# Performance work log

Hardware: AMD Instinct MI355X
Metric: run time of the kernel (lower is better)

Reference implementation:

```python
import jax, jax.numpy as jnp
import numpy as np

C = 256; Ca = C // 2; WH = 8; WW = 8; K = 3; NH = 8; HD = Ca // NH
EPS_LN = 1e-5; EPS_BN = 1e-5

def _rel_pos_idx(wh, ww):
    coords = np.stack(np.meshgrid(np.arange(wh), np.arange(ww), indexing='ij'))  # (2,wh,ww)
    flat = coords.reshape(2, -1)
    rel = (flat[:, :, None] - flat[:, None, :]).transpose(1, 2, 0).astype(np.int64)  # (N,N,2)
    rel[..., 0] += wh - 1
    rel[..., 1] += ww - 1
    rel[..., 0] *= 2 * ww - 1
    return jnp.asarray(rel.sum(-1))  # (N,N)

REL_IDX = _rel_pos_idx(WH, WW)

def _ln(x, g, b):
    m = x.mean(-1, keepdims=True)
    v = x.var(-1, keepdims=True)
    return (x - m) / jnp.sqrt(v + EPS_LN) * g + b

def _bn(x, g, b):  # eval-mode BN, running_mean=0, running_var=1; x is NCHW
    return x * (g / np.sqrt(1.0 + EPS_BN))[None, :, None, None] + b[None, :, None, None]

def _conv1x1(x, w, b):  # w: (O, I)
    return jnp.einsum('bchw,oc->bohw', x, w) + b[None, :, None, None]

def _rwp(x, h, w, wh, ww):  # windows (B*nW, wh*ww, c) -> image (B, c, h, w)
    Bn, N, c = x.shape
    nh, nw = h // wh, w // ww
    B = Bn // (nh * nw)
    x = x.reshape(B, nh, nw, wh, ww, c)
    return x.transpose(0, 5, 1, 3, 2, 4).reshape(B, c, h, w)

def _wp(x, wh, ww):  # image (B, c, h, w) -> windows (B*nW, wh*ww, c)
    B, c, h, w = x.shape
    x = x.reshape(B, c, h // wh, wh, w // ww, ww)
    return x.transpose(0, 2, 4, 3, 5, 1).reshape(-1, wh * ww, c)

def _gelu(t):
    return jax.nn.gelu(t, approximate=False)

def forward(x, rel_pos_bias, attn_w, attn_b, attn_ln_g, attn_ln_b,
            conv_w, conv_b, conv_bn_g, conv_bn_b,
            ci_w1, ci_b1, ci_bn_g, ci_bn_b, ci_w2, ci_b2,
            pr_w, pr_b, cn_bn_g, cn_bn_b,
            qkv_w, qkv_b,
            si_w1, si_b1, si_bn_g, si_bn_b, si_w2, si_b2,
            an_g, an_b, out_w, out_b, h, w):
    B_, N, Cfull = x.shape
    x_attn = _ln(x @ attn_w + attn_b, attn_ln_g, attn_ln_b)  # (B_, N, Ca)
    # conv branch -- note: source applies RWP to raw x (proj_cnn output is dead code)
    x_img = _rwp(x, h, w, WH, WW)  # (B, C, h, w)
    pad = K // 2
    x_cnn = jax.lax.conv_general_dilated(
        x_img, conv_w, (1, 1), [(pad, pad), (pad, pad)],
        dimension_numbers=('NCHW', 'OIHW', 'NCHW'), feature_group_count=Cfull)
    x_cnn = _gelu(_bn(x_cnn + conv_b[None, :, None, None], conv_bn_g, conv_bn_b))
    gap = x_cnn.mean((2, 3), keepdims=True)  # (B, C, 1, 1)
    ci = _conv1x1(gap, ci_w1, ci_b1)
    ci = _gelu(_bn(ci, ci_bn_g, ci_bn_b))
    ci = _conv1x1(ci, ci_w2, ci_b2)  # (B, Ca, 1, 1)
    x_cnn = _conv1x1(x_cnn, pr_w, pr_b)  # (B, Ca, h, w)
    # windowed attention
    qkv = (x_attn @ qkv_w + qkv_b).reshape(B_, N, 3, NH, HD).transpose(2, 0, 3, 1, 4)
    q, k, v = qkv[0], qkv[1], qkv[2]  # each (B_, NH, N, HD)
    B = ci.shape[0]
    ci_s = jax.nn.sigmoid(ci).reshape(B, 1, NH, 1, HD)
    v = (v.reshape(B, B_ // B, NH, N, HD) * ci_s).reshape(B_, NH, N, HD)
    scale = HD ** -0.5
    attn = jnp.einsum('bhnd,bhmd->bhnm', q * scale, k)
    bias = rel_pos_bias[REL_IDX]  # (N, N, NH)
    attn = jax.nn.softmax(attn + bias.transpose(2, 0, 1)[None], axis=-1)
    x_attn = jnp.einsum('bhnm,bhmd->bhnd', attn, v).transpose(0, 2, 1, 3).reshape(B_, N, Ca)
    # spatial interaction gating of conv branch
    x_sp = _rwp(x_attn, h, w, WH, WW)  # (B, Ca, h, w)
    si = _conv1x1(x_sp, si_w1, si_b1)
    si = _gelu(_bn(si, si_bn_g, si_bn_b))
    si = _conv1x1(si, si_w2, si_b2)  # (B, 1, h, w)
    x_cnn = jax.nn.sigmoid(si * x_cnn)
    x_cnn = _bn(x_cnn, cn_bn_g, cn_bn_b)
    x_cnn = _wp(x_cnn, WH, WW)  # (B_, N, Ca)
    x_attn = _ln(x_attn, an_g, an_b)
    return jnp.concatenate([x_attn, x_cnn], axis=-1) @ out_w + out_b

def setup_inputs() -> dict:
    key = jax.random.key(0)
    ks = jax.random.split(key, 12)
    B_, N = 2048, WH * WW
    s = 0.02
    return dict(
        x=jax.random.normal(ks[0], (B_, N, C), jnp.float32),
        rel_pos_bias=jax.random.uniform(ks[1], ((2 * WH - 1) * (2 * WW - 1), NH), jnp.float32),
        attn_w=jax.random.normal(ks[2], (C, Ca)) * s, attn_b=jnp.zeros((Ca,)),
        attn_ln_g=jnp.ones((Ca,)), attn_ln_b=jnp.zeros((Ca,)),
        conv_w=jax.random.normal(ks[3], (C, 1, K, K)) * s, conv_b=jnp.zeros((C,)),
        conv_bn_g=jnp.ones((C,)), conv_bn_b=jnp.zeros((C,)),
        ci_w1=jax.random.normal(ks[4], (C // 8, C)) * s, ci_b1=jnp.zeros((C // 8,)),
        ci_bn_g=jnp.ones((C // 8,)), ci_bn_b=jnp.zeros((C // 8,)),
        ci_w2=jax.random.normal(ks[5], (Ca, C // 8)) * s, ci_b2=jnp.zeros((Ca,)),
        pr_w=jax.random.normal(ks[6], (Ca, C)) * s, pr_b=jnp.zeros((Ca,)),
        cn_bn_g=jnp.ones((Ca,)), cn_bn_b=jnp.zeros((Ca,)),
        qkv_w=jax.random.normal(ks[7], (Ca, 3 * Ca)) * s, qkv_b=jnp.zeros((3 * Ca,)),
        si_w1=jax.random.normal(ks[8], (C // 16, Ca)) * s, si_b1=jnp.zeros((C // 16,)),
        si_bn_g=jnp.ones((C // 16,)), si_bn_b=jnp.zeros((C // 16,)),
        si_w2=jax.random.normal(ks[9], (1, C // 16)) * s, si_b2=jnp.zeros((1,)),
        an_g=jnp.ones((Ca,)), an_b=jnp.zeros((Ca,)),
        out_w=jax.random.normal(ks[10], (C, C)) * s, out_b=jnp.zeros((C,)),
        h=64, w=64,
    )

def reference(x, rel_pos_bias, attn_w, attn_b, attn_ln_g, attn_ln_b,
              conv_w, conv_b, conv_bn_g, conv_bn_b,
              ci_w1, ci_b1, ci_bn_g, ci_bn_b, ci_w2, ci_b2,
              pr_w, pr_b, cn_bn_g, cn_bn_b,
              qkv_w, qkv_b,
              si_w1, si_b1, si_bn_g, si_bn_b, si_w2, si_b2,
              an_g, an_b, out_w, out_b, h, w):
    return forward(x, rel_pos_bias, attn_w, attn_b, attn_ln_g, attn_ln_b,
                   conv_w, conv_b, conv_bn_g, conv_bn_b,
                   ci_w1, ci_b1, ci_bn_g, ci_bn_b, ci_w2, ci_b2,
                   pr_w, pr_b, cn_bn_g, cn_bn_b,
                   qkv_w, qkv_b,
                   si_w1, si_b1, si_bn_g, si_bn_b, si_w2, si_b2,
                   an_g, an_b, out_w, out_b, h, w)
```

## Files before the change

### kernel.cpp

```cpp
#include <hip/hip_runtime.h>
#include <math.h>


#define BNR 0.9999950000374998f

typedef __attribute__((ext_vector_type(8))) short short8;
typedef __attribute__((ext_vector_type(4))) float f32x4;
typedef __attribute__((ext_vector_type(4))) _Float16 half4;
typedef __attribute__((ext_vector_type(8))) _Float16 half8;
typedef __attribute__((ext_vector_type(2))) _Float16 h2v;

__device__ __forceinline__ float gelu_f(float x) {
  const float z = x * (1.0f + 0.044715f * x * x);
  return x / (1.0f + __expf(-1.5957691216057308f * z));
}
__device__ __forceinline__ unsigned short f2bf(float f) {
  unsigned int u = __builtin_bit_cast(unsigned int, f);
  u += 0x7fffu + ((u >> 16) & 1u);
  return (unsigned short)(u >> 16);
}
__device__ __forceinline__ float bf2f(unsigned short h) {
  unsigned int u = ((unsigned int)h) << 16;
  return __builtin_bit_cast(float, u);
}
__device__ __forceinline__ void ld8(const unsigned short* p, float* o) {
  const short8 v = *(const short8*)p;
#pragma unroll
  for (int i = 0; i < 8; ++i) o[i] = bf2f((unsigned short)v[i]);
}
__device__ __forceinline__ unsigned int pkh(float a, float b) {
  return __builtin_bit_cast(unsigned int, __builtin_amdgcn_cvt_pkrtz(a, b));
}

#define ATI(r, ch) (((r) << 8) + ((((ch) ^ ((r)&7))) << 3))

__global__ __launch_bounds__(256) void kpack(
    const float* __restrict__ aw, const float* __restrict__ qw,
    const float* __restrict__ prw, const float* __restrict__ ow,
    const float* __restrict__ sw1, unsigned short* __restrict__ awp,
    unsigned short* __restrict__ qwp, unsigned short* __restrict__ prwp,
    unsigned short* __restrict__ owp, unsigned short* __restrict__ sw1p) {
  const int b = blockIdx.x;
  const float* src; unsigned short* dst; int fs, K, N, NT, trans, f16o;
  if (b < 64)       { fs = b;       src = aw;  dst = awp;  K = 256; N = 128; NT = 8;  trans = 0; f16o = 0; }
  else if (b < 160) { fs = b - 64;  src = qw;  dst = qwp;  K = 128; N = 384; NT = 24; trans = 0; f16o = 0; }
  else if (b < 224) { fs = b - 160; src = prw; dst = prwp; K = 256; N = 128; NT = 8;  trans = 1; f16o = 1; }
  else if (b < 352) { fs = b - 224; src = ow;  dst = owp;  K = 256; N = 256; NT = 16; trans = 0; f16o = 0; }
  else              { fs = b - 352; src = sw1; dst = sw1p; K = 128; N = 16;  NT = 1;  trans = 1; f16o = 0; }
  const int ks = fs / NT, nt = fs % NT;
  for (int idx = threadIdx.x; idx < 512; idx += 256) {
    const int l = idx >> 3, i = idx & 7;
    const int k = ks * 32 + ((l >> 4) << 3) + i, n = nt * 16 + (l & 15);
    const float v = trans ? src[n * K + k] : src[k * N + n];
    dst[(fs * 64 + l) * 8 + i] =
        f16o ? __builtin_bit_cast(unsigned short, (_Float16)v) : f2bf(v);
  }
}

__global__ __launch_bounds__(256) void kbias(const float* __restrict__ rpb,
                                             unsigned short* __restrict__ bt) {
  const int i = blockIdx.x * 256 + threadIdx.x;
  const int h = i >> 12, n = (i >> 6) & 63, m = i & 63;
  const int ny = n >> 3, nx = n & 7, my = m >> 3, mx = m & 7;
  const float v = rpb[((ny - my + 7) * 15 + (nx - mx + 7)) * 8 + h];
  bt[i] = __builtin_bit_cast(unsigned short, (_Float16)v);
}

__global__ __launch_bounds__(256) void k1_attn_ln(
    const float* __restrict__ x, const unsigned short* __restrict__ awp,
    const float* __restrict__ ab, const float* __restrict__ lg,
    const float* __restrict__ lb, unsigned short* __restrict__ xattn,
    unsigned short* __restrict__ xb) {
  const int tid = threadIdx.x, w = tid >> 6, l = tid & 63;
  const int lr = l & 15, lg4 = l >> 4;
  const int r0 = blockIdx.x * 64 + w * 16;
  const float* xp = x + (size_t)(r0 + lr) * 256 + lg4 * 8;
  unsigned short* xbp = xb + (size_t)(r0 + lr) * 256 + lg4 * 8;
  short8 a[8];
#pragma unroll
  for (int ks = 0; ks < 8; ++ks) {
    const float4 f0 = *(const float4*)(xp + ks * 32);
    const float4 f1 = *(const float4*)(xp + ks * 32 + 4);
    short8 av;
    av[0] = f2bf(f0.x); av[1] = f2bf(f0.y); av[2] = f2bf(f0.z); av[3] = f2bf(f0.w);
    av[4] = f2bf(f1.x); av[5] = f2bf(f1.y); av[6] = f2bf(f1.z); av[7] = f2bf(f1.w);
    a[ks] = av;
    uint4 hv;
    hv.x = pkh(f0.x, f0.y); hv.y = pkh(f0.z, f0.w);
    hv.z = pkh(f1.x, f1.y); hv.w = pkh(f1.z, f1.w);
    *(uint4*)(xbp + ks * 32) = hv;
  }
  f32x4 acc[8];
#pragma unroll
  for (int nt = 0; nt < 8; ++nt) acc[nt] = (f32x4)0.f;
#pragma unroll
  for (int nt = 0; nt < 8; ++nt)
#pragma unroll
    for (int ks = 0; ks < 8; ++ks) {
      const short8 bfr = *(const short8*)(awp + ((ks * 8 + nt) * 64 + l) * 8);
      acc[nt] = __builtin_amdgcn_mfma_f32_16x16x32_bf16(a[ks], bfr, acc[nt], 0, 0, 0);
    }
  float bias[8], gam[8], bet[8];
#pragma unroll
  for (int nt = 0; nt < 8; ++nt) {
    const int col = nt * 16 + lr;
    bias[nt] = ab[col]; gam[nt] = lg[col]; bet[nt] = lb[col];
  }
#pragma unroll
  for (int j = 0; j < 4; ++j) {
    float s = 0.f, qq = 0.f;
#pragma unroll
    for (int nt = 0; nt < 8; ++nt) {
      const float v = acc[nt][j] + bias[nt];
      acc[nt][j] = v; s += v; qq += v * v;
    }
    s += __shfl_xor(s, 1); s += __shfl_xor(s, 2);
    s += __shfl_xor(s, 4); s += __shfl_xor(s, 8);
    qq += __shfl_xor(qq, 1); qq += __shfl_xor(qq, 2);
    qq += __shfl_xor(qq, 4); qq += __shfl_xor(qq, 8);
    const float mean = s * (1.f / 128.f);
    const float var = qq * (1.f / 128.f) - mean * mean;
    const float rstd = rsqrtf(var + 1e-5f);
    const int row = r0 + lg4 * 4 + j;
#pragma unroll
    for (int nt = 0; nt < 8; ++nt)
      xattn[(size_t)row * 128 + nt * 16 + lr] =
          f2bf((acc[nt][j] - mean) * rstd * gam[nt] + bet[nt]);
  }
}

__global__ __launch_bounds__(256) void k25_conv(
    const unsigned short* __restrict__ xb, const float* __restrict__ cw,
    const float* __restrict__ cb, const float* __restrict__ bg,
    const float* __restrict__ bb, const unsigned short* __restrict__ prwp,
    const float* __restrict__ prb, unsigned short* __restrict__ xpr,
    float* __restrict__ gpart) {
  __shared__ unsigned short gl[32][264];
  const int tid = threadIdx.x;
  const int bid = (blockIdx.x & 7) * 512 + (blockIdx.x >> 3);
  const int b = bid >> 7;
  const int y = (bid >> 1) & 63;
  const int xt = (bid & 1) * 32;
  const int w = tid >> 6, l = tid & 63;
  {
    const int c0 = l << 2;
    h2v w01[9], w23[9];
#pragma unroll
    for (int k = 0; k < 9; ++k) {
      w01[k][0] = (_Float16)cw[(c0 + 0) * 9 + k];
      w01[k][1] = (_Float16)cw[(c0 + 1) * 9 + k];
      w23[k][0] = (_Float16)cw[(c0 + 2) * 9 + k];
      w23[k][1] = (_Float16)cw[(c0 + 3) * 9 + k];
    }
    const float4 cbf = *(const float4*)&cb[c0];
    float4 scf = *(const float4*)&bg[c0];
    scf.x *= BNR; scf.y *= BNR; scf.z *= BNR; scf.w *= BNR;
    const float4 sbf = *(const float4*)&bb[c0];
    h2v cb01 = {(_Float16)cbf.x, (_Float16)cbf.y};
    h2v cb23 = {(_Float16)cbf.z, (_Float16)cbf.w};
    h2v sc01 = {(_Float16)scf.x, (_Float16)scf.y};
    h2v sc23 = {(_Float16)scf.z, (_Float16)scf.w};
    h2v sb01 = {(_Float16)sbf.x, (_Float16)sbf.y};
    h2v sb23 = {(_Float16)sbf.z, (_Float16)sbf.w};
    float4 gsum = make_float4(0.f, 0.f, 0.f, 0.f);
    const int px0 = xt + w * 8;
#pragma unroll
    for (int sc2 = 0; sc2 < 2; ++sc2) {
      const int p0 = px0 + sc2 * 4;
      h2v v0[3][6], v1[3][6];
#pragma unroll
      for (int dy = 0; dy < 3; ++dy) {
        const int yy = y + dy - 1;
        const bool vy = (unsigned)yy < 64u;
        const int ybase = vy ? ((b * 64 + (yy >> 3) * 8) * 64 + (yy & 7) * 8) : 0;
#pragma unroll
        for (int q = 0; q < 6; ++q) {
          const int xx = p0 - 1 + q;
          h2v a = (h2v)(_Float16)0.f, c = (h2v)(_Float16)0.f;
          if (vy && (unsigned)xx < 64u) {
            const int row = ybase + (xx >> 3) * 64 + (xx & 7);
            const uint2 u = *(const uint2*)&xb[(size_t)row * 256 + c0];
            a = __builtin_bit_cast(h2v, u.x);
            c = __builtin_bit_cast(h2v, u.y);
          }
          v0[dy][q] = a; v1[dy][q] = c;
        }
      }
#pragma unroll
      for (int p = 0; p < 4; ++p) {
        h2v s0 = cb01, s1 = cb23;
#pragma unroll
        for (int dy = 0; dy < 3; ++dy)
#pragma unroll
          for (int dx = 0; dx < 3; ++dx) {
            s0 = w01[dy * 3 + dx] * v0[dy][p + dx] + s0;
            s1 = w23[dy * 3 + dx] * v1[dy][p + dx] + s1;
          }
        s0 = s0 * sc01 + sb01;
        s1 = s1 * sc23 + sb23;
        const float g0 = gelu_f((float)s0[0]), g1 = gelu_f((float)s0[1]);
        const float g2 = gelu_f((float)s1[0]), g3 = gelu_f((float)s1[1]);
        uint2 pk;
        pk.x = pkh(g0, g1); pk.y = pkh(g2, g3);
        *(uint2*)&gl[w * 8 + sc2 * 4 + p][c0] = pk;
        gsum.x += g0; gsum.y += g1; gsum.z += g2; gsum.w += g3;
      }
    }
    *(float4*)&gpart[(size_t)bid * 256 + c0] = gsum;
  }
  __syncthreads();
  const int lr = l & 15, lg4 = l >> 4;
  const int mr0 = (w & 1) * 16, nt0 = (w >> 1) * 4;
  half8 a[8];
#pragma unroll
  for (int ks = 0; ks < 8; ++ks)
    a[ks] = __builtin_bit_cast(half8,
                               *(const short8*)&gl[mr0 + lr][ks * 32 + lg4 * 8]);
  f32x4 acc[4];
#pragma unroll
  for (int nt = 0; nt < 4; ++nt) acc[nt] = (f32x4)0.f;
#pragma unroll
  for (int nt = 0; nt < 4; ++nt)
#pragma unroll
    for (int ks = 0; ks < 8; ++ks) {
      const half8 bfr = __builtin_bit_cast(
          half8, *(const short8*)(prwp + ((ks * 8 + nt0 + nt) * 64 + l) * 8));
      acc[nt] = __builtin_amdgcn_mfma_f32_16x16x32_f16(a[ks], bfr, acc[nt], 0, 0, 0);
    }
#pragma unroll
  for (int nt = 0; nt < 4; ++nt) {
    const int col = (nt0 + nt) * 16 + lr;
    const float bv = prb[col];
#pragma unroll
    for (int j = 0; j < 4; ++j) {
      const int pix = (b * 64 + y) * 64 + xt + mr0 + lg4 * 4 + j;
      xpr[(size_t)pix * 128 + col] = f2bf(acc[nt][j] + bv);
    }
  }
}

__global__ __launch_bounds__(128) void k3_ci(
    const float* __restrict__ gp, const float* __restrict__ w1,
    const float* __restrict__ b1, const float* __restrict__ g1,
    const float* __restrict__ bb1, const float* __restrict__ w2,
    const float* __restrict__ b2, float* __restrict__ cis) {
  __shared__ float gm[256];
  __shared__ float c1[32];
  const int b = blockIdx.x, tid = threadIdx.x;
  for (int c = tid; c < 256; c += 128) {
    float s = 0.f;
    for (int p = 0; p < 128; ++p) s += gp[(size_t)(b * 128 + p) * 256 + c];
    gm[c] = s * (1.f / 4096.f);
  }
  __syncthreads();
  if (tid < 32) {
    float s = b1[tid];
    for (int c = 0; c < 256; ++c) s = fmaf(gm[c], w1[tid * 256 + c], s);
    s = s * (g1[tid] * BNR) + bb1[tid];
    c1[tid] = gelu_f(s);
  }
  __syncthreads();
  float s = b2[tid];
#pragma unroll
  for (int i = 0; i < 32; ++i) s = fmaf(c1[i], w2[tid * 32 + i], s);
  cis[b * 128 + tid] = 1.f / (1.f + __expf(-s));
}

__global__ __launch_bounds__(256, 4) void k4_attn(
    const unsigned short* __restrict__ xa, const unsigned short* __restrict__ qwp,
    const float* __restrict__ qb, const float* __restrict__ cis,
    const unsigned short* __restrict__ biasT, unsigned short* __restrict__ attn) {
  __shared__ _Float16 QS[4][64][38];
  __shared__ _Float16 KS[4][64][38];
  const int tid = threadIdx.x;
  const int win = blockIdx.x, img = win >> 6;
  const int w = tid >> 6, l = tid & 63, lr = l & 15, lg4 = l >> 4;
  {
    float qbv[4];
#pragma unroll
    for (int t = 0; t < 4; ++t) {
      const int gnt = (t < 2) ? (2 * w + t) : (8 + 2 * w + t - 2);
      qbv[t] = qb[gnt * 16 + lr];
    }
    f32x4 acc[4][4];
#pragma unroll
    for (int mt = 0; mt < 4; ++mt)
#pragma unroll
      for (int t = 0; t < 4; ++t) acc[mt][t] = (f32x4)0.f;
#pragma unroll
    for (int ks = 0; ks < 4; ++ks) {
      short8 a[4];
#pragma unroll
      for (int mt = 0; mt < 4; ++mt)
        a[mt] = *(const short8*)(xa + (size_t)(win * 64 + mt * 16 + lr) * 128 +
                                 ks * 32 + lg4 * 8);
#pragma unroll
      for (int t = 0; t < 4; ++t) {
        const int gnt = (t < 2) ? (2 * w + t) : (8 + 2 * w + t - 2);
        const short8 bfr = *(const short8*)(qwp + ((ks * 24 + gnt) * 64 + l) * 8);
#pragma unroll
        for (int mt = 0; mt < 4; ++mt)
          acc[mt][t] = __builtin_amdgcn_mfma_f32_16x16x32_bf16(a[mt], bfr,
                                                               acc[mt][t], 0, 0, 0);
      }
    }
#pragma unroll
    for (int mt = 0; mt < 4; ++mt)
#pragma unroll
      for (int t = 0; t < 4; ++t)
#pragma unroll
        for (int j = 0; j < 4; ++j) {
          const int row = mt * 16 + lg4 * 4 + j;
          const float v = acc[mt][t][j] + qbv[t];
          if (t < 2) QS[w][row][t * 16 + lr] = (_Float16)(v * 0.25f);
          else KS[w][row][(t - 2) * 16 + lr] = (_Float16)v;
        }
  }
  half4 bV2[2][4];
  {
    float qbv[2], cisv[2];
#pragma unroll
    for (int t = 0; t < 2; ++t) {
      qbv[t] = qb[(16 + 2 * w + t) * 16 + lr];
      cisv[t] = cis[img * 128 + (2 * w + t) * 16 + lr];
    }
    f32x4 accv[4][2];
#pragma unroll
    for (int mt = 0; mt < 4; ++mt)
#pragma unroll
      for (int t = 0; t < 2; ++t) accv[mt][t] = (f32x4)0.f;
#pragma unroll
    for (int ks = 0; ks < 4; ++ks) {
      short8 a[4];
#pragma unroll
      for (int mt = 0; mt < 4; ++mt)
        a[mt] = *(const short8*)(xa + (size_t)(win * 64 + mt * 16 + lr) * 128 +
                                 ks * 32 + lg4 * 8);
#pragma unroll
      for (int t = 0; t < 2; ++t) {
        const short8 bfr =
            *(const short8*)(qwp + ((ks * 24 + 16 + 2 * w + t) * 64 + l) * 8);
#pragma unroll
        for (int mt = 0; mt < 4; ++mt)
          accv[mt][t] = __builtin_amdgcn_mfma_f32_16x16x32_bf16(a[mt], bfr,
                                                                accv[mt][t], 0, 0, 0);
      }
    }
#pragma unroll
    for (int t = 0; t < 2; ++t)
#pragma unroll
      for (int kt = 0; kt < 4; ++kt) {
        half4 p;
#pragma unroll
        for (int i = 0; i < 4; ++i)
          p[i] = (_Float16)((accv[kt][t][i] + qbv[t]) * cisv[t]);
        bV2[t][kt] = p;
      }
  }
  for (int hi = 0; hi < 2; ++hi) {
    const int h = w * 2 + hi;
    half4 aK[4], bQ[4];
#pragma unroll
    for (int mt = 0; mt < 4; ++mt)
      aK[mt] = *(const half4*)&KS[w][mt * 16 + lr][hi * 16 + lg4 * 4];
#pragma unroll
    for (int nt = 0; nt < 4; ++nt)
      bQ[nt] = *(const half4*)&QS[w][nt * 16 + lr][hi * 16 + lg4 * 4];
    f32x4 s[4][4];
#pragma unroll
    for (int mt = 0; mt < 4; ++mt)
#pragma unroll
      for (int nt = 0; nt < 4; ++nt)
        s[mt][nt] = __builtin_amdgcn_mfma_f32_16x16x16f16(aK[mt], bQ[nt],
                                                          (f32x4)0.f, 0, 0, 0);
#pragma unroll
    for (int nt = 0; nt < 4; ++nt) {
      const int n = nt * 16 + lr;
      const unsigned short* bp = biasT + (((h << 6) + n) << 6);
#pragma unroll
      for (int mt = 0; mt < 4; ++mt) {
        const half4 b4 = *(const half4*)(bp + mt * 16 + lg4 * 4);
        s[mt][nt][0] += (float)b4[0];
        s[mt][nt][1] += (float)b4[1];
        s[mt][nt][2] += (float)b4[2];
        s[mt][nt][3] += (float)b4[3];
      }
    }
    float inv[4];
#pragma unroll
    for (int nt = 0; nt < 4; ++nt) {
      float m0 = -1e30f;
#pragma unroll
      for (int mt = 0; mt < 4; ++mt)
#pragma unroll
        for (int r = 0; r < 4; ++r) m0 = fmaxf(m0, s[mt][nt][r]);
      m0 = fmaxf(m0, __shfl_xor(m0, 16));
      m0 = fmaxf(m0, __shfl_xor(m0, 32));
      float d0 = 0.f;
#pragma unroll
      for (int mt = 0; mt < 4; ++mt)
#pragma unroll
        for (int r = 0; r < 4; ++r) {
          const float e = __expf(s[mt][nt][r] - m0);
          s[mt][nt][r] = e;
          d0 += e;
        }
      d0 += __shfl_xor(d0, 16);
      d0 += __shfl_xor(d0, 32);
      inv[nt] = 1.f / d0;
    }
    half4 pa[4][4];
#pragma unroll
    for (int nt = 0; nt < 4; ++nt)
#pragma unroll
      for (int kt = 0; kt < 4; ++kt) {
        half4 p;
#pragma unroll
        for (int r = 0; r < 4; ++r) p[r] = (_Float16)(s[kt][nt][r] * inv[nt]);
        pa[nt][kt] = p;
      }
    f32x4 o[4];
#pragma unroll
    for (int nt = 0; nt < 4; ++nt) o[nt] = (f32x4)0.f;
#pragma unroll
    for (int nt = 0; nt < 4; ++nt)
#pragma unroll
      for (int kt = 0; kt < 4; ++kt)
        o[nt] = __builtin_amdgcn_mfma_f32_16x16x16f16(pa[nt][kt], bV2[hi][kt],
                                                      o[nt], 0, 0, 0);
#pragma unroll
    for (int nt = 0; nt < 4; ++nt)
#pragma unroll
      for (int r = 0; r < 4; ++r) {
        const int token = win * 64 + nt * 16 + lg4 * 4 + r;
        attn[(size_t)token * 128 + h * 16 + lr] = f2bf(o[nt][r]);
      }
  }
}

__global__ __launch_bounds__(256) void k6_tail(
    const unsigned short* __restrict__ attn, const unsigned short* __restrict__ xpr,
    const unsigned short* __restrict__ sw1p, const float* __restrict__ sb1,
    const float* __restrict__ sgc, const float* __restrict__ sbc,
    const float* __restrict__ sw2, const float* __restrict__ sb2,
    const float* __restrict__ cg, const float* __restrict__ cbb,
    const float* __restrict__ ag, const float* __restrict__ abb,
    const unsigned short* __restrict__ owp, const float* __restrict__ ob,
    float* __restrict__ out) {
  __shared__ unsigned short At[64 * 256];
  __shared__ float sifl[64];
  __shared__ float statl[64][2];
  const int tid = threadIdx.x;
  const int R0 = blockIdx.x * 64;
  const int w = tid >> 6, l = tid & 63, lr = l & 15, lg4 = l >> 4;
  for (int i = tid; i < 1024; i += 256) {
    const int r = i >> 4, c16 = i & 15;
    *(uint4*)&At[ATI(r, c16)] =
        *(const uint4*)&attn[(size_t)(R0 + r) * 128 + c16 * 8];
    const int R = R0 + r, win = R >> 6, tt = R & 63;
    const int bimg = win >> 6, wy = (win >> 3) & 7, wx = win & 7;
    const int pix = (bimg * 64 + wy * 8 + (tt >> 3)) * 64 + wx * 8 + (tt & 7);
    *(uint4*)&At[ATI(r, 16 + c16)] =
        *(const uint4*)&xpr[(size_t)pix * 128 + c16 * 8];
  }
  __syncthreads();
  {
    const int r = tid >> 2, q = tid & 3;
    float xv[32];
#pragma unroll
    for (int b8 = 0; b8 < 4; ++b8) ld8(&At[ATI(r, q * 4 + b8)], xv + b8 * 8);
    float ps = 0.f, pq = 0.f;
#pragma unroll
    for (int j = 0; j < 32; ++j) { ps += xv[j]; pq += xv[j] * xv[j]; }
    ps += __shfl_xor(ps, 1); ps += __shfl_xor(ps, 2);
    pq += __shfl_xor(pq, 1); pq += __shfl_xor(pq, 2);
    if (q == 0) {
      const float mean = ps * (1.f / 128.f);
      const float var = pq * (1.f / 128.f) - mean * mean;
      statl[r][0] = mean;
      statl[r][1] = rsqrtf(var + 1e-5f);
    }
  }
  {
    const int row = w * 16 + lr;
    f32x4 sa = (f32x4)0.f;
#pragma unroll
    for (int ks = 0; ks < 4; ++ks) {
      const short8 a4 = *(const short8*)&At[ATI(row, ks * 4 + lg4)];
      const short8 bfr = *(const short8*)(sw1p + (ks * 64 + l) * 8);
      sa = __builtin_amdgcn_mfma_f32_16x16x32_bf16(a4, bfr, sa, 0, 0, 0);
    }
    const float sb1v = sb1[lr], g1v = sgc[lr] * BNR, b1v = sbc[lr];
    const float w2v = sw2[lr], sb2v = sb2[0];
#pragma unroll
    for (int j = 0; j < 4; ++j) {
      float s = (sa[j] + sb1v) * g1v + b1v;
      float p = gelu_f(s) * w2v;
      p += __shfl_xor(p, 1); p += __shfl_xor(p, 2);
      p += __shfl_xor(p, 4); p += __shfl_xor(p, 8);
      if (lr == 0) sifl[w * 16 + lg4 * 4 + j] = p + sb2v;
    }
  }
  __syncthreads();
  {
    const int c = tid & 127;
    const float agv = ag[c], abbv = abb[c];
    const float cgv = cg[c] * BNR, cbbv = cbb[c];
#pragma unroll
    for (int k = 0; k < 32; ++k) {
      const int r = (tid >> 7) + k * 2;
      const int ia = ATI(r, c >> 3) + (c & 7);
      const int ic = ATI(r, 16 + (c >> 3)) + (c & 7);
      float a = bf2f(At[ia]);
      a = (a - statl[r][0]) * statl[r][1] * agv + abbv;
      At[ia] = f2bf(a);
      const float cv = bf2f(At[ic]);
      const float g = 1.f / (1.f + __expf(-sifl[r] * cv));
      At[ic] = f2bf(g * cgv + cbbv);
    }
  }
  __syncthreads();
  const int row = w * 16 + lr;
  short8 a[8];
#pragma unroll
  for (int ks = 0; ks < 8; ++ks)
    a[ks] = *(const short8*)&At[ATI(row, ks * 4 + lg4)];
  f32x4 acc[16];
#pragma unroll
  for (int nt = 0; nt < 16; ++nt) acc[nt] = (f32x4)0.f;
#pragma unroll
  for (int nt = 0; nt < 16; ++nt)
#pragma unroll
    for (int ks = 0; ks < 8; ++ks) {
      const short8 bfr = *(const short8*)(owp + ((ks * 16 + nt) * 64 + l) * 8);
      acc[nt] = __builtin_amdgcn_mfma_f32_16x16x32_bf16(a[ks], bfr, acc[nt], 0, 0, 0);
    }
#pragma unroll
  for (int nt = 0; nt < 16; ++nt) {
    const int col = nt * 16 + lr;
    const float bv = ob[col];
#pragma unroll
    for (int j = 0; j < 4; ++j)
      out[(size_t)(R0 + w * 16 + lg4 * 4 + j) * 256 + col] = acc[nt][j] + bv;
  }
}

extern "C" void kernel_launch(void* const* d_in, const int* in_sizes, int n_in,
                              void* d_out, int out_size, void* d_ws,
                              size_t ws_size, hipStream_t stream) {
  (void)in_sizes; (void)n_in; (void)out_size; (void)ws_size;
  const float* x      = (const float*)d_in[0];
  const float* rpb    = (const float*)d_in[1];
  const float* attn_w = (const float*)d_in[2];
  const float* attn_b = (const float*)d_in[3];
  const float* aln_g  = (const float*)d_in[4];
  const float* aln_b  = (const float*)d_in[5];
  const float* conv_w = (const float*)d_in[6];
  const float* conv_b = (const float*)d_in[7];
  const float* cbn_g  = (const float*)d_in[8];
  const float* cbn_b  = (const float*)d_in[9];
  const float* ci_w1  = (const float*)d_in[10];
  const float* ci_b1  = (const float*)d_in[11];
  const float* ci_bg  = (const float*)d_in[12];
  const float* ci_bb  = (const float*)d_in[13];
  const float* ci_w2  = (const float*)d_in[14];
  const float* ci_b2  = (const float*)d_in[15];
  const float* pr_w   = (const float*)d_in[16];
  const float* pr_b   = (const float*)d_in[17];
  const float* cn_g   = (const float*)d_in[18];
  const float* cn_b   = (const float*)d_in[19];
  const float* qkv_w  = (const float*)d_in[20];
  const float* qkv_b  = (const float*)d_in[21];
  const float* si_w1  = (const float*)d_in[22];
  const float* si_b1  = (const float*)d_in[23];
  const float* si_bg  = (const float*)d_in[24];
  const float* si_bb  = (const float*)d_in[25];
  const float* si_w2  = (const float*)d_in[26];
  const float* si_b2  = (const float*)d_in[27];
  const float* an_g   = (const float*)d_in[28];
  const float* an_b   = (const float*)d_in[29];
  const float* out_w  = (const float*)d_in[30];
  const float* out_b  = (const float*)d_in[31];

  unsigned short* xb    = (unsigned short*)d_ws;
  unsigned short* xattn = xb + 33554432;
  unsigned short* attn  = xattn + 16777216;
  unsigned short* xpr   = attn + 16777216;
  float* gpart = (float*)(xpr + 16777216);
  float* cis   = gpart + 1048576;
  unsigned short* awp   = (unsigned short*)(cis + 4096);
  unsigned short* qwp   = awp + 32768;
  unsigned short* prwp  = qwp + 49152;
  unsigned short* owp   = prwp + 32768;
  unsigned short* sw1p  = owp + 65536;
  unsigned short* biasT = sw1p + 2048;

  kpack<<<356, 256, 0, stream>>>(attn_w, qkv_w, pr_w, out_w, si_w1,
                                 awp, qwp, prwp, owp, sw1p);
  kbias<<<128, 256, 0, stream>>>(rpb, biasT);
  k1_attn_ln<<<2048, 256, 0, stream>>>(x, awp, attn_b, aln_g, aln_b, xattn, xb);
  k25_conv<<<4096, 256, 0, stream>>>(xb, conv_w, conv_b, cbn_g, cbn_b, prwp,
                                     pr_b, xpr, gpart);
  k3_ci<<<32, 128, 0, stream>>>(gpart, ci_w1, ci_b1, ci_bg, ci_bb, ci_w2,
                                ci_b2, cis);
  k4_attn<<<2048, 256, 0, stream>>>(xattn, qwp, qkv_b, cis, biasT, attn);
  k6_tail<<<2048, 256, 0, stream>>>(attn, xpr, sw1p, si_b1, si_bg, si_bb,
                                    si_w2, si_b2, cn_g, cn_b, an_g, an_b,
                                    owp, out_b, (float*)d_out);
}
```

Before: 300.2 us.

## Fuse window attention with tail projection kernel and fold bias table into pack

Merges the attention kernel and the tail kernel (spatial interaction, norms, output projection) into one per-window kernel. The attention output now goes straight into a shared-memory tile instead of a bf16 global buffer, which removes a full write and re-read of the attention intermediate and one launch. The bias-table kernel is also folded into the weight-pack launch. The fused kernel reuses one shared buffer for Q/K staging and the tail tile, and preloads the xpr rows into registers early. That raises register pressure under the 4-blocks-per-SM launch bound and could lower occupancy or cause spills.

```diff
diff --git a/kernel.cpp b/kernel.cpp
--- a/kernel.cpp
+++ b/kernel.cpp
@@ -37,10 +37,19 @@
 __global__ __launch_bounds__(256) void kpack(
     const float* __restrict__ aw, const float* __restrict__ qw,
     const float* __restrict__ prw, const float* __restrict__ ow,
-    const float* __restrict__ sw1, unsigned short* __restrict__ awp,
-    unsigned short* __restrict__ qwp, unsigned short* __restrict__ prwp,
-    unsigned short* __restrict__ owp, unsigned short* __restrict__ sw1p) {
+    const float* __restrict__ sw1, const float* __restrict__ rpb,
+    unsigned short* __restrict__ awp, unsigned short* __restrict__ qwp,
+    unsigned short* __restrict__ prwp, unsigned short* __restrict__ owp,
+    unsigned short* __restrict__ sw1p, unsigned short* __restrict__ bt) {
   const int b = blockIdx.x;
+  if (b >= 356) {
+    const int i = (b - 356) * 256 + threadIdx.x;
+    const int h = i >> 12, n = (i >> 6) & 63, m = i & 63;
+    const int ny = n >> 3, nx = n & 7, my = m >> 3, mx = m & 7;
+    const float v = rpb[((ny - my + 7) * 15 + (nx - mx + 7)) * 8 + h];
+    bt[i] = __builtin_bit_cast(unsigned short, (_Float16)v);
+    return;
+  }
   const float* src; unsigned short* dst; int fs, K, N, NT, trans, f16o;
   if (b < 64)       { fs = b;       src = aw;  dst = awp;  K = 256; N = 128; NT = 8;  trans = 0; f16o = 0; }
   else if (b < 160) { fs = b - 64;  src = qw;  dst = qwp;  K = 128; N = 384; NT = 24; trans = 0; f16o = 0; }
@@ -55,15 +64,6 @@
     dst[(fs * 64 + l) * 8 + i] =
         f16o ? __builtin_bit_cast(unsigned short, (_Float16)v) : f2bf(v);
   }
-}
-
-__global__ __launch_bounds__(256) void kbias(const float* __restrict__ rpb,
-                                             unsigned short* __restrict__ bt) {
-  const int i = blockIdx.x * 256 + threadIdx.x;
-  const int h = i >> 12, n = (i >> 6) & 63, m = i & 63;
-  const int ny = n >> 3, nx = n & 7, my = m >> 3, mx = m & 7;
-  const float v = rpb[((ny - my + 7) * 15 + (nx - mx + 7)) * 8 + h];
-  bt[i] = __builtin_bit_cast(unsigned short, (_Float16)v);
 }
 
 __global__ __launch_bounds__(256) void k1_attn_ln(
@@ -266,15 +266,35 @@
   cis[b * 128 + tid] = 1.f / (1.f + __expf(-s));
 }
 
-__global__ __launch_bounds__(256, 4) void k4_attn(
+__global__ __launch_bounds__(256, 4) void k46_attn_tail(
     const unsigned short* __restrict__ xa, const unsigned short* __restrict__ qwp,
     const float* __restrict__ qb, const float* __restrict__ cis,
-    const unsigned short* __restrict__ biasT, unsigned short* __restrict__ attn) {
-  __shared__ _Float16 QS[4][64][38];
-  __shared__ _Float16 KS[4][64][38];
+    const unsigned short* __restrict__ biasT, const unsigned short* __restrict__ xpr,
+    const unsigned short* __restrict__ sw1p, const float* __restrict__ sb1,
+    const float* __restrict__ sgc, const float* __restrict__ sbc,
+    const float* __restrict__ sw2, const float* __restrict__ sb2,
+    const float* __restrict__ cg, const float* __restrict__ cbb,
+    const float* __restrict__ ag, const float* __restrict__ abb,
+    const unsigned short* __restrict__ owp, const float* __restrict__ ob,
+    float* __restrict__ out) {
+  __shared__ __align__(16) unsigned char Ubuf[35840];
+  __shared__ float sifl[64];
+  __shared__ float statl[64][2];
+  _Float16(*QS)[64][36] = reinterpret_cast<_Float16(*)[64][36]>(Ubuf);
+  _Float16(*KS)[64][34] = reinterpret_cast<_Float16(*)[64][34]>(Ubuf + 18432);
+  unsigned short* At = (unsigned short*)Ubuf;
   const int tid = threadIdx.x;
   const int win = blockIdx.x, img = win >> 6;
   const int w = tid >> 6, l = tid & 63, lr = l & 15, lg4 = l >> 4;
+  const int wy = (win >> 3) & 7, wx = win & 7;
+  uint4 xr[4];
+#pragma unroll
+  for (int kk = 0; kk < 4; ++kk) {
+    const int i = tid + kk * 256;
+    const int r = i >> 4, c16 = i & 15;
+    const int pix = (img * 64 + wy * 8 + (r >> 3)) * 64 + wx * 8 + (r & 7);
+    xr[kk] = *(const uint4*)&xpr[(size_t)pix * 128 + c16 * 8];
+  }
   {
     float qbv[4];
 #pragma unroll
@@ -357,6 +377,7 @@
         bV2[t][kt] = p;
       }
   }
+  f32x4 o[2][4];
   for (int hi = 0; hi < 2; ++hi) {
     const int h = w * 2 + hi;
     half4 aK[4], bQ[4];
@@ -419,49 +440,32 @@
         for (int r = 0; r < 4; ++r) p[r] = (_Float16)(s[kt][nt][r] * inv[nt]);
         pa[nt][kt] = p;
       }
-    f32x4 o[4];
-#pragma unroll
-    for (int nt = 0; nt < 4; ++nt) o[nt] = (f32x4)0.f;
+#pragma unroll
+    for (int nt = 0; nt < 4; ++nt) o[hi][nt] = (f32x4)0.f;
 #pragma unroll
     for (int nt = 0; nt < 4; ++nt)
 #pragma unroll
       for (int kt = 0; kt < 4; ++kt)
-        o[nt] = __builtin_amdgcn_mfma_f32_16x16x16f16(pa[nt][kt], bV2[hi][kt],
-                                                      o[nt], 0, 0, 0);
+        o[hi][nt] = __builtin_amdgcn_mfma_f32_16x16x16f16(pa[nt][kt], bV2[hi][kt],
+                                                          o[hi][nt], 0, 0, 0);
+  }
+  __syncthreads();
+#pragma unroll
+  for (int hi = 0; hi < 2; ++hi) {
+    const int ch = w * 4 + hi * 2 + (lr >> 3), co = lr & 7;
 #pragma unroll
     for (int nt = 0; nt < 4; ++nt)
 #pragma unroll
       for (int r = 0; r < 4; ++r) {
-        const int token = win * 64 + nt * 16 + lg4 * 4 + r;
-        attn[(size_t)token * 128 + h * 16 + lr] = f2bf(o[nt][r]);
-      }
-  }
-}
-
-__global__ __launch_bounds__(256) void k6_tail(
-    const unsigned short* __restrict__ attn, const unsigned short* __restrict__ xpr,
-    const unsigned short* __restrict__ sw1p, const float* __restrict__ sb1,
-    const float* __restrict__ sgc, const float* __restrict__ sbc,
-    const float* __restrict__ sw2, const float* __restrict__ sb2,
-    const float* __restrict__ cg, const float* __restrict__ cbb,
-    const float* __restrict__ ag, const float* __restrict__ abb,
-    const unsigned short* __restrict__ owp, const float* __restrict__ ob,
-    float* __restrict__ out) {
-  __shared__ unsigned short At[64 * 256];
-  __shared__ float sifl[64];
-  __shared__ float statl[64][2];
-  const int tid = threadIdx.x;
-  const int R0 = blockIdx.x * 64;
-  const int w = tid >> 6, l = tid & 63, lr = l & 15, lg4 = l >> 4;
-  for (int i = tid; i < 1024; i += 256) {
+        const int token = nt * 16 + lg4 * 4 + r;
+        At[ATI(token, ch) + co] = f2bf(o[hi][nt][r]);
+      }
+  }
+#pragma unroll
+  for (int kk = 0; kk < 4; ++kk) {
+    const int i = tid + kk * 256;
     const int r = i >> 4, c16 = i & 15;
-    *(uint4*)&At[ATI(r, c16)] =
-        *(const uint4*)&attn[(size_t)(R0 + r) * 128 + c16 * 8];
-    const int R = R0 + r, win = R >> 6, tt = R & 63;
-    const int bimg = win >> 6, wy = (win >> 3) & 7, wx = win & 7;
-    const int pix = (bimg * 64 + wy * 8 + (tt >> 3)) * 64 + wx * 8 + (tt & 7);
-    *(uint4*)&At[ATI(r, 16 + c16)] =
-        *(const uint4*)&xpr[(size_t)pix * 128 + c16 * 8];
+    *(uint4*)&At[ATI(r, 16 + c16)] = xr[kk];
   }
   __syncthreads();
   {
@@ -521,10 +525,10 @@
   }
   __syncthreads();
   const int row = w * 16 + lr;
-  short8 a[8];
+  short8 af[8];
 #pragma unroll
   for (int ks = 0; ks < 8; ++ks)
-    a[ks] = *(const short8*)&At[ATI(row, ks * 4 + lg4)];
+    af[ks] = *(const short8*)&At[ATI(row, ks * 4 + lg4)];
   f32x4 acc[16];
 #pragma unroll
   for (int nt = 0; nt < 16; ++nt) acc[nt] = (f32x4)0.f;
@@ -533,7 +537,7 @@
 #pragma unroll
     for (int ks = 0; ks < 8; ++ks) {
       const short8 bfr = *(const short8*)(owp + ((ks * 16 + nt) * 64 + l) * 8);
-      acc[nt] = __builtin_amdgcn_mfma_f32_16x16x32_bf16(a[ks], bfr, acc[nt], 0, 0, 0);
+      acc[nt] = __builtin_amdgcn_mfma_f32_16x16x32_bf16(af[ks], bfr, acc[nt], 0, 0, 0);
     }
 #pragma unroll
   for (int nt = 0; nt < 16; ++nt) {
@@ -541,7 +545,7 @@
     const float bv = ob[col];
 #pragma unroll
     for (int j = 0; j < 4; ++j)
-      out[(size_t)(R0 + w * 16 + lg4 * 4 + j) * 256 + col] = acc[nt][j] + bv;
+      out[(size_t)(win * 64 + w * 16 + lg4 * 4 + j) * 256 + col] = acc[nt][j] + bv;
   }
 }
 
@@ -584,8 +588,7 @@
 
   unsigned short* xb    = (unsigned short*)d_ws;
   unsigned short* xattn = xb + 33554432;
-  unsigned short* attn  = xattn + 16777216;
-  unsigned short* xpr   = attn + 16777216;
+  unsigned short* xpr   = xattn + 16777216;
   float* gpart = (float*)(xpr + 16777216);
   float* cis   = gpart + 1048576;
   unsigned short* awp   = (unsigned short*)(cis + 4096);
@@ -595,16 +598,14 @@
   unsigned short* sw1p  = owp + 65536;
   unsigned short* biasT = sw1p + 2048;
 
-  kpack<<<356, 256, 0, stream>>>(attn_w, qkv_w, pr_w, out_w, si_w1,
-                                 awp, qwp, prwp, owp, sw1p);
-  kbias<<<128, 256, 0, stream>>>(rpb, biasT);
+  kpack<<<484, 256, 0, stream>>>(attn_w, qkv_w, pr_w, out_w, si_w1, rpb,
+                                 awp, qwp, prwp, owp, sw1p, biasT);
   k1_attn_ln<<<2048, 256, 0, stream>>>(x, awp, attn_b, aln_g, aln_b, xattn, xb);
   k25_conv<<<4096, 256, 0, stream>>>(xb, conv_w, conv_b, cbn_g, cbn_b, prwp,
                                      pr_b, xpr, gpart);
   k3_ci<<<32, 128, 0, stream>>>(gpart, ci_w1, ci_b1, ci_bg, ci_bb, ci_w2,
                                 ci_b2, cis);
-  k4_attn<<<2048, 256, 0, stream>>>(xattn, qwp, qkv_b, cis, biasT, attn);
-  k6_tail<<<2048, 256, 0, stream>>>(attn, xpr, sw1p, si_b1, si_bg, si_bb,
-                                    si_w2, si_b2, cn_g, cn_b, an_g, an_b,
-                                    owp, out_b, (float*)d_out);
-}
+  k46_attn_tail<<<2048, 256, 0, stream>>>(
+      xattn, qwp, qkv_b, cis, biasT, xpr, sw1p, si_b1, si_bg, si_bb, si_w2,
+      si_b2, cn_g, cn_b, an_g, an_b, owp, out_b, (float*)d_out);
+}
```

New measurement: 291.1 us. -3.0%, faster.
